# Kernel optimization log

Hardware: AMD Instinct MI355X
Metric: run time of the kernel (lower is better)

Reference implementation:

```python
import jax, jax.numpy as jnp
import numpy as np

D_MODEL = 1024
EPS = 1e-5  # torch LayerNorm default


def layernorm(x, gamma, beta):
    mu = jnp.mean(x, axis=-1, keepdims=True)
    var = jnp.mean(jnp.square(x - mu), axis=-1, keepdims=True)
    return (x - mu) * jax.lax.rsqrt(var + EPS) * gamma + beta


def setup_inputs() -> dict:
    key = jax.random.key(0)
    ks = jax.random.split(key, 9)
    B, S, D = 4, 2048, D_MODEL
    s = 1.0 / np.sqrt(D)  # ~ nn.Linear default init scale
    return {
        "x": jax.random.normal(ks[0], (B, S, D), dtype=jnp.float32),
        "wq_w": jax.random.uniform(ks[1], (D, D), jnp.float32, -s, s),
        "wq_b": jax.random.uniform(ks[2], (D,), jnp.float32, -s, s),
        "wk_w": jax.random.uniform(ks[3], (D, D), jnp.float32, -s, s),
        "wk_b": jax.random.uniform(ks[4], (D,), jnp.float32, -s, s),
        "wv_w": jax.random.uniform(ks[5], (D, D), jnp.float32, -s, s),
        "wv_b": jax.random.uniform(ks[6], (D,), jnp.float32, -s, s),
        "lin_w": jax.random.uniform(ks[7], (D, D), jnp.float32, -s, s),
        "lin_b": jax.random.uniform(ks[8], (D,), jnp.float32, -s, s),
        "g1": jnp.ones((D,), jnp.float32),
        "b1": jnp.zeros((D,), jnp.float32),
        "g2": jnp.ones((D,), jnp.float32),
        "b2": jnp.zeros((D,), jnp.float32),
    }


def reference(x, wq_w, wq_b, wk_w, wk_b, wv_w, wv_b, lin_w, lin_b, g1, b1, g2, b2):
    # single-head attention over full d_model (num_heads unused in original forward)
    q = jnp.einsum("bsd,ed->bse", x, wq_w) + wq_b
    k = jnp.einsum("bsd,ed->bse", x, wk_w) + wk_b
    v = jnp.einsum("bsd,ed->bse", x, wv_w) + wv_b
    scale = 1.0 / jnp.sqrt(jnp.float32(x.shape[-1]))
    scores = jax.nn.softmax(jnp.einsum("bqd,bkd->bqk", q, k) * scale, axis=2)
    attention = jnp.einsum("bqk,bkd->bqd", scores, v)
    # faithful to original: tril applied to the [S, D] attention OUTPUT per batch
    attention = jnp.tril(attention)
    x = layernorm(x + attention, g1, b1)
    linear_output = jnp.einsum("bsd,ed->bse", x, lin_w) + lin_b
    x = layernorm(x + linear_output, g2, b2)
    return x
```

## Files before the change

### kernel.cpp

```cpp
#include <hip/hip_runtime.h>
#include <hip/hip_bf16.h>

#define SEQ 2048
#define DM 1024
#define NB 4

typedef short bf16x8 __attribute__((ext_vector_type(8)));
typedef float f32x4 __attribute__((ext_vector_type(4)));
typedef float f32x4v __attribute__((ext_vector_type(4)));
typedef unsigned short u16x4 __attribute__((ext_vector_type(4)));
typedef unsigned short u16x8 __attribute__((ext_vector_type(8)));

__device__ __forceinline__ float bf2f(unsigned short u) {
  union { unsigned int i; float f; } w; w.i = ((unsigned int)u) << 16; return w.f;
}
__device__ __forceinline__ unsigned short f2bf(float f) {
  union { __hip_bfloat16 h; unsigned short u; } w; w.h = __float2bfloat16(f); return w.u;
}
__device__ __forceinline__ void load_lds16(const void* g, void* l) {
  __builtin_amdgcn_global_load_lds((const __attribute__((address_space(1))) void*)g,
                                   (__attribute__((address_space(3))) void*)l, 16, 0, 0);
}
__device__ __forceinline__ void cvt4(const float* __restrict__ in,
                                     unsigned short* __restrict__ out, int i) {
  f32x4v v = ((const f32x4v*)in)[i];
  u16x4 o;
  o[0] = f2bf(v[0]); o[1] = f2bf(v[1]); o[2] = f2bf(v[2]); o[3] = f2bf(v[3]);
  ((u16x4*)out)[i] = o;
}

__global__ __launch_bounds__(256) void stage_kernel(
    const float* __restrict__ x,
    const float* __restrict__ wq, const float* __restrict__ wk,
    const float* __restrict__ wv, const float* __restrict__ lw,
    const float* __restrict__ bq, const float* __restrict__ bk, const float* __restrict__ bv,
    unsigned short* __restrict__ xb, unsigned short* __restrict__ wqkvb,
    unsigned short* __restrict__ lwb, float* __restrict__ bqkv)
{
  const int XC = (NB * SEQ * DM) / 4;
  const int WC = (DM * DM) / 4;
  const int BC = (3 * DM) / 4;
  const int total = XC + 4 * WC + BC;
  int idx = blockIdx.x * 256 + threadIdx.x;
  int stride = gridDim.x * 256;
  for (int i = idx; i < total; i += stride) {
    if (i < XC) { cvt4(x, xb, i); continue; }
    int j = i - XC;
    if (j < WC)          { cvt4(wq, wqkvb, j); continue; }
    if (j < 2 * WC)      { cvt4(wk, wqkvb + (size_t)DM * DM, j - WC); continue; }
    if (j < 3 * WC)      { cvt4(wv, wqkvb + 2 * (size_t)DM * DM, j - 2 * WC); continue; }
    if (j < 4 * WC)      { cvt4(lw, lwb, j - 3 * WC); continue; }
    int c = j - 4 * WC;
    const float* src = (c < 256) ? bq : ((c < 512) ? bk : bv);
    int off = (c < 256) ? c : ((c < 512) ? c - 256 : c - 512);
    ((f32x4v*)bqkv)[c] = ((const f32x4v*)src)[off];
  }
}

__global__ __launch_bounds__(256, 2) void gemm_bt(
    const unsigned short* __restrict__ A, int lda, long sA,
    const unsigned short* __restrict__ B, int ldb, long sB,
    void* __restrict__ Cv, int ldc, long sC,
    int K, const float* __restrict__ bias, float scale, int outf32, int trilskip)
{
  const int m0 = blockIdx.x * 128, n0 = blockIdx.y * 128;
  if (trilskip && n0 > m0 + 127) return;
  __shared__ unsigned short As[128 * 64];
  __shared__ unsigned short Bs[128 * 64];
  const int tid = threadIdx.x;
  const int lane = tid & 63;
  const int wave = tid >> 6;
  const int wm = wave >> 1, wn = wave & 1;
  const unsigned short* Ab = A + (size_t)sA * blockIdx.z;
  const unsigned short* Bb = B + (size_t)sB * blockIdx.z;

  f32x4 acc[4][4];
#pragma unroll
  for (int i = 0; i < 4; ++i)
#pragma unroll
    for (int j = 0; j < 4; ++j)
      acc[i][j] = (f32x4){0.f, 0.f, 0.f, 0.f};

  const int nk = K >> 6;
  for (int kt = 0; kt < nk; ++kt) {
    __syncthreads();
    const int kb = kt << 6;
#pragma unroll
    for (int it = 0; it < 4; ++it) {
      int c = it * 256 + tid;
      int row = c >> 3;
      int lslot = (c & 7) ^ (row & 7);
      int ldsoff = (it * 256 + wave * 64) * 8;
      load_lds16(Ab + (size_t)(m0 + row) * lda + kb + lslot * 8, &As[ldsoff]);
      load_lds16(Bb + (size_t)(n0 + row) * ldb + kb + lslot * 8, &Bs[ldsoff]);
    }
    __syncthreads();
#pragma unroll
    for (int h = 0; h < 2; ++h) {
      bf16x8 af[4], bfr[4];
#pragma unroll
      for (int i = 0; i < 4; ++i) {
        int row = wm * 64 + i * 16 + (lane & 15);
        int pslot = (h * 4 + (lane >> 4)) ^ (row & 7);
        af[i] = *(const bf16x8*)&As[row * 64 + pslot * 8];
      }
#pragma unroll
      for (int j = 0; j < 4; ++j) {
        int row = wn * 64 + j * 16 + (lane & 15);
        int pslot = (h * 4 + (lane >> 4)) ^ (row & 7);
        bfr[j] = *(const bf16x8*)&Bs[row * 64 + pslot * 8];
      }
#pragma unroll
      for (int i = 0; i < 4; ++i)
#pragma unroll
        for (int j = 0; j < 4; ++j)
          acc[i][j] = __builtin_amdgcn_mfma_f32_16x16x32_bf16(af[i], bfr[j], acc[i][j], 0, 0, 0);
    }
  }

  const int rsub = (lane >> 4) * 4;
  const int cbase = n0 + wn * 64 + (lane & 15);
  if (outf32) {
    float* C = (float*)Cv + (size_t)sC * blockIdx.z;
#pragma unroll
    for (int i = 0; i < 4; ++i) {
      int rbase = m0 + wm * 64 + i * 16 + rsub;
#pragma unroll
      for (int j = 0; j < 4; ++j)
#pragma unroll
        for (int r = 0; r < 4; ++r)
          C[(size_t)(rbase + r) * ldc + cbase + j * 16] = acc[i][j][r] * scale;
    }
  } else {
    unsigned short* C = (unsigned short*)Cv + (size_t)sC * blockIdx.z;
    float bv[4] = {0.f, 0.f, 0.f, 0.f};
    if (bias) {
#pragma unroll
      for (int j = 0; j < 4; ++j) bv[j] = bias[cbase + j * 16];
    }
#pragma unroll
    for (int i = 0; i < 4; ++i) {
      int rbase = m0 + wm * 64 + i * 16 + rsub;
#pragma unroll
      for (int j = 0; j < 4; ++j)
#pragma unroll
        for (int r = 0; r < 4; ++r)
          C[(size_t)(rbase + r) * ldc + cbase + j * 16] = f2bf(acc[i][j][r] * scale + bv[j]);
    }
  }
}

__global__ __launch_bounds__(512, 2) void gemm256(
    const unsigned short* __restrict__ A, int lda, long sA,
    const unsigned short* __restrict__ B, int ldb, long sB,
    void* __restrict__ Cv, int ldc, long sC,
    int K, const float* __restrict__ bias, float scale, int outf32,
    unsigned short* __restrict__ vtOut, int vtBase)
{
  __shared__ unsigned short As[2][256 * 64];
  __shared__ unsigned short Bs[2][256 * 64];
  const int tid = threadIdx.x;
  const int lane = tid & 63;
  const int wave = tid >> 6;
  const int wm = wave >> 2;
  const int wn = wave & 3;
  const int m0 = blockIdx.x * 256, n0 = blockIdx.y * 256;
  const unsigned short* Ab = A + (size_t)sA * blockIdx.z;
  const unsigned short* Bb = B + (size_t)sB * blockIdx.z;

  f32x4 acc[8][4];
#pragma unroll
  for (int i = 0; i < 8; ++i)
#pragma unroll
    for (int j = 0; j < 4; ++j)
      acc[i][j] = (f32x4){0.f, 0.f, 0.f, 0.f};

  const int nk = K >> 6;

  auto STAGE = [&](int b, int kt) {
    const int kb = kt << 6;
#pragma unroll
    for (int i = 0; i < 4; ++i) {
      int c = i * 512 + tid;
      int row = c >> 3;
      int lslot = (c & 7) ^ (row & 7);
      load_lds16(Ab + (size_t)(m0 + row) * lda + kb + lslot * 8, &As[b][c * 8]);
      load_lds16(Bb + (size_t)(n0 + row) * ldb + kb + lslot * 8, &Bs[b][c * 8]);
    }
  };

  STAGE(0, 0);
  if (nk > 1) {
    STAGE(1, 1);
    asm volatile("s_waitcnt vmcnt(8)" ::: "memory");
  } else {
    asm volatile("s_waitcnt vmcnt(0)" ::: "memory");
  }
  __builtin_amdgcn_sched_barrier(0);
  __builtin_amdgcn_s_barrier();
  __builtin_amdgcn_sched_barrier(0);

  for (int kt = 0; kt < nk; ++kt) {
    const int b = kt & 1;
    const unsigned short* Asb = As[b];
    const unsigned short* Bsb = Bs[b];
    bf16x8 bfr[4][2];
#pragma unroll
    for (int j = 0; j < 4; ++j) {
      int row = wn * 64 + j * 16 + (lane & 15);
#pragma unroll
      for (int h = 0; h < 2; ++h) {
        int pslot = (h * 4 + (lane >> 4)) ^ (row & 7);
        bfr[j][h] = *(const bf16x8*)&Bsb[row * 64 + pslot * 8];
      }
    }
#pragma unroll
    for (int q = 0; q < 4; ++q) {
      bf16x8 af[2][2];
#pragma unroll
      for (int i = 0; i < 2; ++i) {
        int row = wm * 128 + (q * 2 + i) * 16 + (lane & 15);
#pragma unroll
        for (int h = 0; h < 2; ++h) {
          int pslot = (h * 4 + (lane >> 4)) ^ (row & 7);
          af[i][h] = *(const bf16x8*)&Asb[row * 64 + pslot * 8];
        }
      }
      __builtin_amdgcn_s_setprio(1);
#pragma unroll
      for (int i = 0; i < 2; ++i)
#pragma unroll
        for (int j = 0; j < 4; ++j)
#pragma unroll
          for (int h = 0; h < 2; ++h)
            acc[q * 2 + i][j] =
                __builtin_amdgcn_mfma_f32_16x16x32_bf16(af[i][h], bfr[j][h], acc[q * 2 + i][j], 0, 0, 0);
      __builtin_amdgcn_s_setprio(0);
    }
    __builtin_amdgcn_sched_barrier(0);
    __builtin_amdgcn_s_barrier();
    __builtin_amdgcn_sched_barrier(0);
    if (kt + 2 < nk) STAGE(b, kt + 2);
    if (kt + 1 < nk) {
      if (kt + 2 < nk) asm volatile("s_waitcnt vmcnt(8)" ::: "memory");
      else             asm volatile("s_waitcnt vmcnt(0)" ::: "memory");
      __builtin_amdgcn_sched_barrier(0);
      __builtin_amdgcn_s_barrier();
      __builtin_amdgcn_sched_barrier(0);
    }
  }

  const int rsub = (lane >> 4) * 4;
  const int cbase = n0 + wn * 64 + (lane & 15);
  if (vtOut && n0 >= vtBase) {
    float bv[4] = {0.f, 0.f, 0.f, 0.f};
    if (bias) {
#pragma unroll
      for (int j = 0; j < 4; ++j) bv[j] = bias[cbase + j * 16];
    }
#pragma unroll
    for (int i = 0; i < 8; ++i) {
      int sg = m0 + wm * 128 + i * 16 + rsub;
      int bb = sg >> 11;
      int sl = sg & (SEQ - 1);
#pragma unroll
      for (int j = 0; j < 4; ++j) {
        int d = cbase + j * 16 - vtBase;
        u16x4 o;
#pragma unroll
        for (int r = 0; r < 4; ++r) o[r] = f2bf(acc[i][j][r] * scale + bv[j]);
        *(u16x4*)&vtOut[((size_t)bb * DM + d) * SEQ + sl] = o;
      }
    }
  } else if (outf32) {
    float* C = (float*)Cv + (size_t)sC * blockIdx.z;
#pragma unroll
    for (int i = 0; i < 8; ++i) {
      int rbase = m0 + wm * 128 + i * 16 + rsub;
#pragma unroll
      for (int j = 0; j < 4; ++j)
#pragma unroll
        for (int r = 0; r < 4; ++r)
          C[(size_t)(rbase + r) * ldc + cbase + j * 16] = acc[i][j][r] * scale;
    }
  } else {
    unsigned short* C = (unsigned short*)Cv + (size_t)sC * blockIdx.z;
    float bv[4] = {0.f, 0.f, 0.f, 0.f};
    if (bias) {
#pragma unroll
      for (int j = 0; j < 4; ++j) bv[j] = bias[cbase + j * 16];
    }
#pragma unroll
    for (int i = 0; i < 8; ++i) {
      int rbase = m0 + wm * 128 + i * 16 + rsub;
#pragma unroll
      for (int j = 0; j < 4; ++j)
#pragma unroll
        for (int r = 0; r < 4; ++r)
          C[(size_t)(rbase + r) * ldc + cbase + j * 16] = f2bf(acc[i][j][r] * scale + bv[j]);
    }
  }
}

__global__ __launch_bounds__(256) void softmax_kernel(unsigned short* __restrict__ Sc) {
  int row = blockIdx.x;
  int tid = threadIdx.x;
  unsigned short* sr = Sc + (size_t)row * SEQ;
  u16x8 raw = *(const u16x8*)&sr[tid * 8];
  float v[8];
#pragma unroll
  for (int j = 0; j < 8; ++j) v[j] = bf2f(raw[j]);
  float m = v[0];
#pragma unroll
  for (int j = 1; j < 8; ++j) m = fmaxf(m, v[j]);
#pragma unroll
  for (int off = 32; off; off >>= 1) m = fmaxf(m, __shfl_xor(m, off));
  __shared__ float red[8];
  int wv = tid >> 6;
  if ((tid & 63) == 0) red[wv] = m;
  __syncthreads();
  m = fmaxf(fmaxf(red[0], red[1]), fmaxf(red[2], red[3]));
  float s = 0.f;
#pragma unroll
  for (int j = 0; j < 8; ++j) { v[j] = __expf(v[j] - m); s += v[j]; }
#pragma unroll
  for (int off = 32; off; off >>= 1) s += __shfl_xor(s, off);
  if ((tid & 63) == 0) red[4 + wv] = s;
  __syncthreads();
  s = red[4] + red[5] + red[6] + red[7];
  float inv = 1.f / s;
  u16x8 o;
#pragma unroll
  for (int j = 0; j < 8; ++j) o[j] = f2bf(v[j] * inv);
  *(u16x8*)&sr[tid * 8] = o;
}

__global__ __launch_bounds__(256) void ln_kernel(
    const float* __restrict__ xf, const unsigned short* __restrict__ xb,
    const unsigned short* __restrict__ res, int masked,
    const float* __restrict__ g, const float* __restrict__ be,
    float* __restrict__ outf, unsigned short* __restrict__ outb)
{
  int row = blockIdx.x;
  int s = row & (SEQ - 1);
  int tid = threadIdx.x;
  int d0 = tid * 4;
  float v[4];
  if (xf) {
    f32x4v t = ((const f32x4v*)(xf + (size_t)row * DM))[tid];
    v[0]=t[0]; v[1]=t[1]; v[2]=t[2]; v[3]=t[3];
  } else {
    u16x4 t = ((const u16x4*)(xb + (size_t)row * DM))[tid];
    v[0]=bf2f(t[0]); v[1]=bf2f(t[1]); v[2]=bf2f(t[2]); v[3]=bf2f(t[3]);
  }
  u16x4 rv = ((const u16x4*)(res + (size_t)row * DM))[tid];
#pragma unroll
  for (int j = 0; j < 4; ++j) {
    float r = bf2f(rv[j]);
    if (masked && (d0 + j) > s) r = 0.f;
    v[j] += r;
  }
  float s1 = v[0] + v[1] + v[2] + v[3];
  float s2 = v[0]*v[0] + v[1]*v[1] + v[2]*v[2] + v[3]*v[3];
#pragma unroll
  for (int off = 32; off; off >>= 1) { s1 += __shfl_xor(s1, off); s2 += __shfl_xor(s2, off); }
  __shared__ float red[8];
  int wv = tid >> 6;
  if ((tid & 63) == 0) { red[wv] = s1; red[4 + wv] = s2; }
  __syncthreads();
  s1 = red[0] + red[1] + red[2] + red[3];
  s2 = red[4] + red[5] + red[6] + red[7];
  float mean = s1 * (1.f / DM);
  float var = s2 * (1.f / DM) - mean * mean;
  float rstd = rsqrtf(var + 1e-5f);
  f32x4v gv = ((const f32x4v*)g)[tid];
  f32x4v bv = ((const f32x4v*)be)[tid];
  if (outf) {
    f32x4v o;
#pragma unroll
    for (int j = 0; j < 4; ++j) o[j] = (v[j] - mean) * rstd * gv[j] + bv[j];
    ((f32x4v*)(outf + (size_t)row * DM))[tid] = o;
  } else {
    u16x4 o;
#pragma unroll
    for (int j = 0; j < 4; ++j) o[j] = f2bf((v[j] - mean) * rstd * gv[j] + bv[j]);
    ((u16x4*)(outb + (size_t)row * DM))[tid] = o;
  }
}

extern "C" void kernel_launch(void* const* d_in, const int* in_sizes, int n_in,
                              void* d_out, int out_size, void* d_ws, size_t ws_size,
                              hipStream_t stream) {
  (void)in_sizes; (void)n_in; (void)out_size; (void)ws_size;
  const float* x     = (const float*)d_in[0];
  const float* wq_w  = (const float*)d_in[1];
  const float* wq_b  = (const float*)d_in[2];
  const float* wk_w  = (const float*)d_in[3];
  const float* wk_b  = (const float*)d_in[4];
  const float* wv_w  = (const float*)d_in[5];
  const float* wv_b  = (const float*)d_in[6];
  const float* lin_w = (const float*)d_in[7];
  const float* lin_b = (const float*)d_in[8];
  const float* g1    = (const float*)d_in[9];
  const float* b1    = (const float*)d_in[10];
  const float* g2    = (const float*)d_in[11];
  const float* b2    = (const float*)d_in[12];

  const size_t MB = 1ull << 20;
  char* ws = (char*)d_ws;
  unsigned short* scP  = (unsigned short*)(ws);
  unsigned short* attn = (unsigned short*)(ws + 32*MB);
  unsigned short* x1   = (unsigned short*)(ws + 48*MB);
  unsigned short* lin  = (unsigned short*)(ws + 64*MB);
  unsigned short* xb   = (unsigned short*)(ws + 80*MB);
  unsigned short* wqkvb= (unsigned short*)(ws + 96*MB);
  unsigned short* lwb  = (unsigned short*)(ws + 102*MB);
  float*          bqkv = (float*)(ws + 104*MB);
  unsigned short* qkv  = (unsigned short*)(ws + 112*MB);
  unsigned short* vt   = (unsigned short*)(ws + 160*MB);

  stage_kernel<<<2048, 256, 0, stream>>>(x, wq_w, wk_w, wv_w, lin_w, wq_b, wk_b, wv_b,
                                         xb, wqkvb, lwb, bqkv);

  gemm256<<<dim3(32, 12, 1), 512, 0, stream>>>(xb, DM, 0, wqkvb, DM, 0, qkv, 3 * DM, 0,
                                               DM, bqkv, 1.f, 0, vt, 2 * DM);

  const float scale = 0.03125f;
  gemm256<<<dim3(8, 8, NB), 512, 0, stream>>>(
      qkv, 3 * DM, (long)SEQ * 3 * DM,
      qkv + DM, 3 * DM, (long)SEQ * 3 * DM,
      scP, SEQ, (long)SEQ * SEQ, DM, nullptr, scale, 0, nullptr, 0);
  softmax_kernel<<<NB * SEQ, 256, 0, stream>>>(scP);
  gemm_bt<<<dim3(16, 8, NB), 256, 0, stream>>>(
      scP, SEQ, (long)SEQ * SEQ,
      vt, SEQ, (long)DM * SEQ,
      attn, DM, (long)SEQ * DM, SEQ, nullptr, 1.f, 0, 1);

  ln_kernel<<<NB * SEQ, 256, 0, stream>>>(nullptr, xb, attn, 1, g1, b1, nullptr, x1);
  gemm_bt<<<dim3(64, 8, 1), 256, 0, stream>>>(x1, DM, 0, lwb, DM, 0, lin, DM, 0, DM, lin_b, 1.f, 0, 0);
  ln_kernel<<<NB * SEQ, 256, 0, stream>>>(nullptr, x1, lin, 0, g2, b2, (float*)d_out, nullptr);
}
```

Measured before the change: 224.4 us.

## Switch QK GEMMs to 256x128 tiles with triple-buffered LDS pipeline

Replaces the 256x256 double-buffered GEMM with a 256x128-tile kernel that keeps three K-stages of A and B in one shared LDS array. The deeper prefetch is meant to hide more global-load latency. The smaller N tile doubles the block count for the QKV projection and the score GEMMs, which should reduce tail imbalance across CUs. In exchange, each tile does less reuse per loaded byte, and the now-unused fp32 output path is removed.

```diff
diff --git a/kernel.cpp b/kernel.cpp
--- a/kernel.cpp
+++ b/kernel.cpp
@@ -150,27 +150,26 @@
   }
 }
 
-__global__ __launch_bounds__(512, 2) void gemm256(
+__global__ __launch_bounds__(512, 2) void gemm_deep(
     const unsigned short* __restrict__ A, int lda, long sA,
     const unsigned short* __restrict__ B, int ldb, long sB,
     void* __restrict__ Cv, int ldc, long sC,
-    int K, const float* __restrict__ bias, float scale, int outf32,
+    int K, const float* __restrict__ bias, float scale,
     unsigned short* __restrict__ vtOut, int vtBase)
 {
-  __shared__ unsigned short As[2][256 * 64];
-  __shared__ unsigned short Bs[2][256 * 64];
+  __shared__ unsigned short lds[3][(256 + 128) * 64];
   const int tid = threadIdx.x;
   const int lane = tid & 63;
   const int wave = tid >> 6;
-  const int wm = wave >> 2;
-  const int wn = wave & 3;
-  const int m0 = blockIdx.x * 256, n0 = blockIdx.y * 256;
+  const int wm = wave >> 1;
+  const int wn = wave & 1;
+  const int m0 = blockIdx.x * 256, n0 = blockIdx.y * 128;
   const unsigned short* Ab = A + (size_t)sA * blockIdx.z;
   const unsigned short* Bb = B + (size_t)sB * blockIdx.z;
 
-  f32x4 acc[8][4];
-#pragma unroll
-  for (int i = 0; i < 8; ++i)
+  f32x4 acc[4][4];
+#pragma unroll
+  for (int i = 0; i < 4; ++i)
 #pragma unroll
     for (int j = 0; j < 4; ++j)
       acc[i][j] = (f32x4){0.f, 0.f, 0.f, 0.f};
@@ -180,30 +179,26 @@
   auto STAGE = [&](int b, int kt) {
     const int kb = kt << 6;
 #pragma unroll
-    for (int i = 0; i < 4; ++i) {
+    for (int i = 0; i < 6; ++i) {
       int c = i * 512 + tid;
       int row = c >> 3;
       int lslot = (c & 7) ^ (row & 7);
-      load_lds16(Ab + (size_t)(m0 + row) * lda + kb + lslot * 8, &As[b][c * 8]);
-      load_lds16(Bb + (size_t)(n0 + row) * ldb + kb + lslot * 8, &Bs[b][c * 8]);
+      const unsigned short* src = (row < 256)
+          ? Ab + (size_t)(m0 + row) * lda + kb + lslot * 8
+          : Bb + (size_t)(n0 + row - 256) * ldb + kb + lslot * 8;
+      load_lds16(src, &lds[b][c * 8]);
     }
   };
 
-  STAGE(0, 0);
-  if (nk > 1) {
-    STAGE(1, 1);
-    asm volatile("s_waitcnt vmcnt(8)" ::: "memory");
-  } else {
-    asm volatile("s_waitcnt vmcnt(0)" ::: "memory");
-  }
+  STAGE(0, 0); STAGE(1, 1); STAGE(2, 2);
+  asm volatile("s_waitcnt vmcnt(12)" ::: "memory");
   __builtin_amdgcn_sched_barrier(0);
   __builtin_amdgcn_s_barrier();
   __builtin_amdgcn_sched_barrier(0);
 
   for (int kt = 0; kt < nk; ++kt) {
-    const int b = kt & 1;
-    const unsigned short* Asb = As[b];
-    const unsigned short* Bsb = Bs[b];
+    const unsigned short* Asb = &lds[kt % 3][0];
+    const unsigned short* Bsb = Asb + 256 * 64;
     bf16x8 bfr[4][2];
 #pragma unroll
     for (int j = 0; j < 4; ++j) {
@@ -215,35 +210,30 @@
       }
     }
 #pragma unroll
-    for (int q = 0; q < 4; ++q) {
-      bf16x8 af[2][2];
-#pragma unroll
-      for (int i = 0; i < 2; ++i) {
-        int row = wm * 128 + (q * 2 + i) * 16 + (lane & 15);
-#pragma unroll
-        for (int h = 0; h < 2; ++h) {
-          int pslot = (h * 4 + (lane >> 4)) ^ (row & 7);
-          af[i][h] = *(const bf16x8*)&Asb[row * 64 + pslot * 8];
-        }
+    for (int i = 0; i < 4; ++i) {
+      bf16x8 af[2];
+      int arow = wm * 64 + i * 16 + (lane & 15);
+#pragma unroll
+      for (int h = 0; h < 2; ++h) {
+        int pslot = (h * 4 + (lane >> 4)) ^ (arow & 7);
+        af[h] = *(const bf16x8*)&Asb[arow * 64 + pslot * 8];
       }
       __builtin_amdgcn_s_setprio(1);
 #pragma unroll
-      for (int i = 0; i < 2; ++i)
-#pragma unroll
-        for (int j = 0; j < 4; ++j)
-#pragma unroll
-          for (int h = 0; h < 2; ++h)
-            acc[q * 2 + i][j] =
-                __builtin_amdgcn_mfma_f32_16x16x32_bf16(af[i][h], bfr[j][h], acc[q * 2 + i][j], 0, 0, 0);
+      for (int j = 0; j < 4; ++j)
+#pragma unroll
+        for (int h = 0; h < 2; ++h)
+          acc[i][j] = __builtin_amdgcn_mfma_f32_16x16x32_bf16(af[h], bfr[j][h], acc[i][j], 0, 0, 0);
       __builtin_amdgcn_s_setprio(0);
     }
     __builtin_amdgcn_sched_barrier(0);
     __builtin_amdgcn_s_barrier();
     __builtin_amdgcn_sched_barrier(0);
-    if (kt + 2 < nk) STAGE(b, kt + 2);
+    if (kt + 3 < nk) STAGE(kt % 3, kt + 3);
     if (kt + 1 < nk) {
-      if (kt + 2 < nk) asm volatile("s_waitcnt vmcnt(8)" ::: "memory");
-      else             asm volatile("s_waitcnt vmcnt(0)" ::: "memory");
+      if (kt + 3 < nk)      asm volatile("s_waitcnt vmcnt(12)" ::: "memory");
+      else if (kt + 2 < nk) asm volatile("s_waitcnt vmcnt(6)"  ::: "memory");
+      else                  asm volatile("s_waitcnt vmcnt(0)"  ::: "memory");
       __builtin_amdgcn_sched_barrier(0);
       __builtin_amdgcn_s_barrier();
       __builtin_amdgcn_sched_barrier(0);
@@ -252,15 +242,15 @@
 
   const int rsub = (lane >> 4) * 4;
   const int cbase = n0 + wn * 64 + (lane & 15);
+  float bv[4] = {0.f, 0.f, 0.f, 0.f};
+  if (bias) {
+#pragma unroll
+    for (int j = 0; j < 4; ++j) bv[j] = bias[cbase + j * 16];
+  }
   if (vtOut && n0 >= vtBase) {
-    float bv[4] = {0.f, 0.f, 0.f, 0.f};
-    if (bias) {
-#pragma unroll
-      for (int j = 0; j < 4; ++j) bv[j] = bias[cbase + j * 16];
-    }
-#pragma unroll
-    for (int i = 0; i < 8; ++i) {
-      int sg = m0 + wm * 128 + i * 16 + rsub;
+#pragma unroll
+    for (int i = 0; i < 4; ++i) {
+      int sg = m0 + wm * 64 + i * 16 + rsub;
       int bb = sg >> 11;
       int sl = sg & (SEQ - 1);
 #pragma unroll
@@ -272,27 +262,11 @@
         *(u16x4*)&vtOut[((size_t)bb * DM + d) * SEQ + sl] = o;
       }
     }
-  } else if (outf32) {
-    float* C = (float*)Cv + (size_t)sC * blockIdx.z;
-#pragma unroll
-    for (int i = 0; i < 8; ++i) {
-      int rbase = m0 + wm * 128 + i * 16 + rsub;
-#pragma unroll
-      for (int j = 0; j < 4; ++j)
-#pragma unroll
-        for (int r = 0; r < 4; ++r)
-          C[(size_t)(rbase + r) * ldc + cbase + j * 16] = acc[i][j][r] * scale;
-    }
   } else {
     unsigned short* C = (unsigned short*)Cv + (size_t)sC * blockIdx.z;
-    float bv[4] = {0.f, 0.f, 0.f, 0.f};
-    if (bias) {
-#pragma unroll
-      for (int j = 0; j < 4; ++j) bv[j] = bias[cbase + j * 16];
-    }
-#pragma unroll
-    for (int i = 0; i < 8; ++i) {
-      int rbase = m0 + wm * 128 + i * 16 + rsub;
+#pragma unroll
+    for (int i = 0; i < 4; ++i) {
+      int rbase = m0 + wm * 64 + i * 16 + rsub;
 #pragma unroll
       for (int j = 0; j < 4; ++j)
 #pragma unroll
@@ -422,14 +396,14 @@
   stage_kernel<<<2048, 256, 0, stream>>>(x, wq_w, wk_w, wv_w, lin_w, wq_b, wk_b, wv_b,
                                          xb, wqkvb, lwb, bqkv);
 
-  gemm256<<<dim3(32, 12, 1), 512, 0, stream>>>(xb, DM, 0, wqkvb, DM, 0, qkv, 3 * DM, 0,
-                                               DM, bqkv, 1.f, 0, vt, 2 * DM);
+  gemm_deep<<<dim3(32, 24, 1), 512, 0, stream>>>(xb, DM, 0, wqkvb, DM, 0, qkv, 3 * DM, 0,
+                                                 DM, bqkv, 1.f, vt, 2 * DM);
 
   const float scale = 0.03125f;
-  gemm256<<<dim3(8, 8, NB), 512, 0, stream>>>(
+  gemm_deep<<<dim3(8, 16, NB), 512, 0, stream>>>(
       qkv, 3 * DM, (long)SEQ * 3 * DM,
       qkv + DM, 3 * DM, (long)SEQ * 3 * DM,
-      scP, SEQ, (long)SEQ * SEQ, DM, nullptr, scale, 0, nullptr, 0);
+      scP, SEQ, (long)SEQ * SEQ, DM, nullptr, scale, nullptr, 0);
   softmax_kernel<<<NB * SEQ, 256, 0, stream>>>(scP);
   gemm_bt<<<dim3(16, 8, NB), 256, 0, stream>>>(
       scP, SEQ, (long)SEQ * SEQ,
@@ -437,6 +411,7 @@
       attn, DM, (long)SEQ * DM, SEQ, nullptr, 1.f, 0, 1);
 
   ln_kernel<<<NB * SEQ, 256, 0, stream>>>(nullptr, xb, attn, 1, g1, b1, nullptr, x1);
-  gemm_bt<<<dim3(64, 8, 1), 256, 0, stream>>>(x1, DM, 0, lwb, DM, 0, lin, DM, 0, DM, lin_b, 1.f, 0, 0);
+  gemm_bt<<<dim3(64, 8, 1), 256, 0, stream>>>(x1, DM, 0, lwb, DM, 0, lin, DM, 0, DM,
+                                              lin_b, 1.f, 0, 0);
   ln_kernel<<<NB * SEQ, 256, 0, stream>>>(nullptr, x1, lin, 0, g2, b2, (float*)d_out, nullptr);
 }
```

New measurement: 223.5 us. About the same (-0.4%).
